# Performance work log

Measured on AMD Instinct MI355X. Metric: run time of the kernel, lower is better.

Reference implementation:

```python
import jax, jax.numpy as jnp
import numpy as np

EPS = 1e-16  # matches torch_geometric softmax denominator guard


def setup_inputs() -> dict:
    E, N, D = 1_600_000, 50_000, 32
    key = jax.random.key(0)
    k1, k2, k3, k4, k5 = jax.random.split(key, 5)
    return {
        "x": jax.random.normal(k1, (E, D), dtype=jnp.float32),
        "attention_x": jax.random.normal(k2, (E, D), dtype=jnp.float32),
        "index": jax.random.randint(k3, (E,), 0, N, dtype=jnp.int32),
        "size": N,
        "W_emb": jax.random.normal(k4, (D, D), dtype=jnp.float32) / np.sqrt(D),
        "b_emb": jnp.zeros((D,), dtype=jnp.float32),
        "W_score": jax.random.normal(k5, (D, 1), dtype=jnp.float32) / np.sqrt(D),
        "b_score": jnp.zeros((1,), dtype=jnp.float32),
    }


def reference(x, attention_x, index, size, W_emb, b_emb, W_score, b_score):
    # embedding_module: per-edge linear transform -> [E, D]
    h = x @ W_emb + b_emb
    # score_module: per-edge scalar score -> [E]
    scores = (attention_x @ W_score + b_score)[:, 0]
    # segment softmax over edges sharing the same target node
    seg_max = jax.ops.segment_max(scores, index, num_segments=size)  # [N]
    ex = jnp.exp(scores - seg_max[index])                            # [E]
    denom = jax.ops.segment_sum(ex, index, num_segments=size)       # [N]
    w = ex / (denom[index] + EPS)                                    # [E]
    # weighted scatter-add aggregation -> [N, D]
    out = jax.ops.segment_sum(h * w[:, None], index, num_segments=size)
    return out
```

## Files before the change

### kernel.cpp

```cpp
#include <hip/hip_runtime.h>

#define DD 32
#define EPSF 1e-16f
#define SCAN_T 1024
#define BSH 5
#define BNODES (1 << BSH)
#define BMAX 2048
#define K3_TPB 256
#define K3_EPT 16
#define K3_EPB (K3_TPB * K3_EPT)
#define CHUNK 1536
#define CPT (CHUNK / 256)

__global__ void score_kernel(const float* __restrict__ ax,
                             const float* __restrict__ Wsf,
                             const float* __restrict__ bsf,
                             float* __restrict__ ex, int E) {
    int i = blockIdx.x * blockDim.x + threadIdx.x;
    int e0 = i * 2;
    if (e0 >= E) return;
    bool two = (e0 + 1 < E);
    int e1 = two ? e0 + 1 : e0;

    const float4* r0 = reinterpret_cast<const float4*>(ax + (size_t)e0 * DD);
    const float4* r1 = reinterpret_cast<const float4*>(ax + (size_t)e1 * DD);
    float b = bsf[0];
    float s0 = b, s1 = b;
#pragma unroll
    for (int q = 0; q < 8; ++q) {
        float4 f0 = r0[q];
        float4 f1 = r1[q];
        float w0 = Wsf[4 * q], w1 = Wsf[4 * q + 1];
        float w2 = Wsf[4 * q + 2], w3 = Wsf[4 * q + 3];
        s0 = fmaf(f0.x, w0, s0); s0 = fmaf(f0.y, w1, s0);
        s0 = fmaf(f0.z, w2, s0); s0 = fmaf(f0.w, w3, s0);
        s1 = fmaf(f1.x, w0, s1); s1 = fmaf(f1.y, w1, s1);
        s1 = fmaf(f1.z, w2, s1); s1 = fmaf(f1.w, w3, s1);
    }
    float ex0 = __expf(s0), ex1 = __expf(s1);
    if (two) reinterpret_cast<float2*>(ex)[i] = make_float2(ex0, ex1);
    else     ex[e0] = ex0;
}

__launch_bounds__(K3_TPB)
__global__ void hist_kernel(const int* __restrict__ index,
                            int* __restrict__ bcnt, int E, int B) {
    __shared__ int lcnt[BMAX];
    int t = threadIdx.x;
    int base = blockIdx.x * K3_EPB;
    int nE = min(K3_EPB, E - base);

    for (int b = t; b < B; b += K3_TPB) lcnt[b] = 0;
    __syncthreads();
    for (int off = t; off < nE; off += K3_TPB)
        atomicAdd(&lcnt[index[base + off] >> BSH], 1);
    __syncthreads();
    for (int b = t; b < B; b += K3_TPB)
        if (lcnt[b]) atomicAdd(&bcnt[b], lcnt[b]);
}

__global__ void scan_kernel(const int* __restrict__ bcnt, int* __restrict__ boff,
                            int* __restrict__ bcursor, int B) {
    __shared__ int part[SCAN_T];
    int t = threadIdx.x;
    int chunk = (B + SCAN_T - 1) / SCAN_T;
    int lo = t * chunk;
    int hi = min(lo + chunk, B);
    int s = 0;
    for (int i = lo; i < hi; ++i) s += bcnt[i];
    part[t] = s;
    __syncthreads();
    for (int d = 1; d < SCAN_T; d <<= 1) {
        int v = (t >= d) ? part[t - d] : 0;
        __syncthreads();
        part[t] += v;
        __syncthreads();
    }
    int run = (t == 0) ? 0 : part[t - 1];
    for (int i = lo; i < hi; ++i) {
        boff[i] = run;
        bcursor[i] = run;
        run += bcnt[i];
    }
    if (t == SCAN_T - 1) boff[B] = run;
}

__launch_bounds__(K3_TPB)
__global__ void bin_kernel(const int* __restrict__ index,
                           const float* __restrict__ ex,
                           int* __restrict__ bcursor,
                           uint2* __restrict__ pairs, int E, int B) {
    __shared__ int lcnt[BMAX];
    __shared__ int lbase[BMAX];
    int t = threadIdx.x;
    int base = blockIdx.x * K3_EPB;
    int nE = min(K3_EPB, E - base);

    for (int b = t; b < B; b += K3_TPB) lcnt[b] = 0;
    __syncthreads();

    int idxv[K3_EPT];
#pragma unroll
    for (int i = 0; i < K3_EPT; ++i) {
        int off = i * K3_TPB + t;
        idxv[i] = -1;
        if (off < nE) {
            idxv[i] = index[base + off];
            atomicAdd(&lcnt[idxv[i] >> BSH], 1);
        }
    }
    __syncthreads();

    for (int b = t; b < B; b += K3_TPB) {
        int c = lcnt[b];
        lbase[b] = (c > 0) ? atomicAdd(&bcursor[b], c) : 0;
        lcnt[b] = 0;
    }
    __syncthreads();

#pragma unroll
    for (int i = 0; i < K3_EPT; ++i) {
        int off = i * K3_TPB + t;
        if (off >= nE) continue;
        int e = base + off;
        float exv = ex[e];
        int idx = idxv[i];
        int b = idx >> BSH;
        int pos = atomicAdd(&lcnt[b], 1);
        pairs[lbase[b] + pos] =
            make_uint2((unsigned)e | ((unsigned)(idx & (BNODES - 1)) << 21),
                       __float_as_uint(exv));
    }
}

__launch_bounds__(256)
__global__ void aggregate_kernel(const float* __restrict__ x,
                                 const uint2* __restrict__ pairs,
                                 const int* __restrict__ boff,
                                 const float* __restrict__ Wf,
                                 const float* __restrict__ bfv,
                                 float* __restrict__ out, int N) {
    __shared__ uint2 sp[CHUNK];
    __shared__ int cnt[BNODES];
    __shared__ int offs[BNODES + 1];
    __shared__ int cur[BNODES];

    int bk = blockIdx.x;
    int nbase = bk << BSH;
    int t = threadIdx.x;
    int wid = t >> 6;
    int lane = t & 63;
    int half = lane >> 5;
    int k = lane & 31;

    int beg = boff[bk], end = boff[bk + 1];

    float yacc[8], dacc[8];
#pragma unroll
    for (int s = 0; s < 8; ++s) { yacc[s] = 0.0f; dacc[s] = 0.0f; }

    for (int cb = beg; cb < end; cb += CHUNK) {
        int csz = min(CHUNK, end - cb);

        uint2 vreg[CPT];
#pragma unroll
        for (int j = 0; j < CPT; ++j) {
            int i = j * 256 + t;
            vreg[j].x = 0xFFFFFFFFu;
            if (i < csz) vreg[j] = pairs[cb + i];
        }

        if (t < BNODES) cnt[t] = 0;
        __syncthreads();
#pragma unroll
        for (int j = 0; j < CPT; ++j)
            if (vreg[j].x != 0xFFFFFFFFu)
                atomicAdd(&cnt[(vreg[j].x >> 21) & (BNODES - 1)], 1);
        __syncthreads();
        if (t == 0) {
            int r = 0;
            for (int n = 0; n < BNODES; ++n) { offs[n] = r; cur[n] = r; r += cnt[n]; }
            offs[BNODES] = r;
        }
        __syncthreads();
#pragma unroll
        for (int j = 0; j < CPT; ++j) {
            if (vreg[j].x != 0xFFFFFFFFu) {
                int nl = (vreg[j].x >> 21) & (BNODES - 1);
                int slot = atomicAdd(&cur[nl], 1);
                sp[slot] = vreg[j];
            }
        }
        __syncthreads();

#pragma unroll
        for (int s = 0; s < 8; ++s) {
            int nl = wid * 8 + s;
            int lo = offs[nl], hi = offs[nl + 1];
            float ya = 0.0f, da = 0.0f;
            int p = lo + half;
            for (; p + 14 < hi; p += 16) {
                uint2 a0 = sp[p],      a1 = sp[p + 2];
                uint2 a2 = sp[p + 4],  a3 = sp[p + 6];
                uint2 a4 = sp[p + 8],  a5 = sp[p + 10];
                uint2 a6 = sp[p + 12], a7 = sp[p + 14];
                float w0 = __uint_as_float(a0.y), w1 = __uint_as_float(a1.y);
                float w2 = __uint_as_float(a2.y), w3 = __uint_as_float(a3.y);
                float w4 = __uint_as_float(a4.y), w5 = __uint_as_float(a5.y);
                float w6 = __uint_as_float(a6.y), w7 = __uint_as_float(a7.y);
                float x0 = x[(size_t)(a0.x & 0x1FFFFFu) * DD + k];
                float x1 = x[(size_t)(a1.x & 0x1FFFFFu) * DD + k];
                float x2 = x[(size_t)(a2.x & 0x1FFFFFu) * DD + k];
                float x3 = x[(size_t)(a3.x & 0x1FFFFFu) * DD + k];
                float x4 = x[(size_t)(a4.x & 0x1FFFFFu) * DD + k];
                float x5 = x[(size_t)(a5.x & 0x1FFFFFu) * DD + k];
                float x6 = x[(size_t)(a6.x & 0x1FFFFFu) * DD + k];
                float x7 = x[(size_t)(a7.x & 0x1FFFFFu) * DD + k];
                ya = fmaf(w0, x0, ya); ya = fmaf(w1, x1, ya);
                ya = fmaf(w2, x2, ya); ya = fmaf(w3, x3, ya);
                ya = fmaf(w4, x4, ya); ya = fmaf(w5, x5, ya);
                ya = fmaf(w6, x6, ya); ya = fmaf(w7, x7, ya);
                da += ((w0 + w1) + (w2 + w3)) + ((w4 + w5) + (w6 + w7));
            }
            for (; p + 6 < hi; p += 8) {
                uint2 a0 = sp[p],     a1 = sp[p + 2];
                uint2 a2 = sp[p + 4], a3 = sp[p + 6];
                float w0 = __uint_as_float(a0.y), w1 = __uint_as_float(a1.y);
                float w2 = __uint_as_float(a2.y), w3 = __uint_as_float(a3.y);
                float x0 = x[(size_t)(a0.x & 0x1FFFFFu) * DD + k];
                float x1 = x[(size_t)(a1.x & 0x1FFFFFu) * DD + k];
                float x2 = x[(size_t)(a2.x & 0x1FFFFFu) * DD + k];
                float x3 = x[(size_t)(a3.x & 0x1FFFFFu) * DD + k];
                ya = fmaf(w0, x0, ya); ya = fmaf(w1, x1, ya);
                ya = fmaf(w2, x2, ya); ya = fmaf(w3, x3, ya);
                da += (w0 + w1) + (w2 + w3);
            }
            for (; p < hi; p += 2) {
                uint2 a = sp[p];
                float w = __uint_as_float(a.y);
                ya = fmaf(w, x[(size_t)(a.x & 0x1FFFFFu) * DD + k], ya);
                da += w;
            }
            yacc[s] += ya;
            dacc[s] += da;
        }
        __syncthreads();
    }

#pragma unroll
    for (int s = 0; s < 8; ++s) {
        float ya = yacc[s] + __shfl_xor(yacc[s], 32);
        float da = dacc[s] + __shfl_xor(dacc[s], 32);
        int node = nbase + wid * 8 + s;
        if (node < N) {
            float inv = 1.0f / (da + EPSF);
            float yn = ya * inv;
            float sw = da * inv;
            float o = sw * bfv[k];
#pragma unroll
            for (int kk = 0; kk < DD; ++kk)
                o = fmaf(__shfl(yn, kk), Wf[kk * DD + k], o);
            if (half == 0) out[(size_t)node * DD + k] = o;
        }
    }
}

extern "C" void kernel_launch(void* const* d_in, const int* in_sizes, int n_in,
                              void* d_out, int out_size, void* d_ws, size_t ws_size,
                              hipStream_t stream) {
    const float* x       = (const float*)d_in[0];
    const float* ax      = (const float*)d_in[1];
    const int*   index   = (const int*)d_in[2];
    const float* W_emb   = (const float*)d_in[4];
    const float* b_emb   = (const float*)d_in[5];
    const float* W_score = (const float*)d_in[6];
    const float* b_score = (const float*)d_in[7];

    int E = in_sizes[0] / DD;
    int N = out_size / DD;
    int B = (N + BNODES - 1) >> BSH;

    uint2* pairs   = (uint2*)d_ws;
    float* ex      = (float*)(pairs + (size_t)E);
    int*   bcnt    = (int*)(ex + (size_t)E);
    int*   boff    = bcnt + B;
    int*   bcursor = boff + B + 1;

    hipMemsetAsync(bcnt, 0, sizeof(int) * (size_t)B, stream);

    int blocksE2 = ((E + 1) / 2 + 255) / 256;
    score_kernel<<<blocksE2, 256, 0, stream>>>(ax, W_score, b_score, ex, E);

    int blocksK = (E + K3_EPB - 1) / K3_EPB;
    hist_kernel<<<blocksK, K3_TPB, 0, stream>>>(index, bcnt, E, B);
    scan_kernel<<<1, SCAN_T, 0, stream>>>(bcnt, boff, bcursor, B);
    bin_kernel<<<blocksK, K3_TPB, 0, stream>>>(index, ex, bcursor, pairs, E, B);
    aggregate_kernel<<<B, 256, 0, stream>>>(x, pairs, boff, W_emb, b_emb,
                                            (float*)d_out, N);
}
```

Before: 184.6 us.

## Fuse score and histogram kernels; replace serial bucket prefix with wave scan

Merges the per-edge score/exp computation with the bucket histogram into one kernel, with each thread handling four consecutive edges. This removes a launch and an extra pass over the index array. The single-thread 32-entry prefix sum in the aggregate kernel becomes a shuffle-based scan across 32 lanes. In exchange, each thread now reads strided float4 rows (four edges per thread, non-coalesced across lanes), and every 1024-edge block must zero and flush a 2048-entry shared histogram, which means many more global atomics than the old 4096-edge blocks.

```diff
diff --git a/kernel.cpp b/kernel.cpp
--- a/kernel.cpp
+++ b/kernel.cpp
@@ -11,51 +11,72 @@
 #define K3_EPB (K3_TPB * K3_EPT)
 #define CHUNK 1536
 #define CPT (CHUNK / 256)
-
-__global__ void score_kernel(const float* __restrict__ ax,
-                             const float* __restrict__ Wsf,
-                             const float* __restrict__ bsf,
-                             float* __restrict__ ex, int E) {
-    int i = blockIdx.x * blockDim.x + threadIdx.x;
-    int e0 = i * 2;
-    if (e0 >= E) return;
-    bool two = (e0 + 1 < E);
-    int e1 = two ? e0 + 1 : e0;
-
-    const float4* r0 = reinterpret_cast<const float4*>(ax + (size_t)e0 * DD);
-    const float4* r1 = reinterpret_cast<const float4*>(ax + (size_t)e1 * DD);
-    float b = bsf[0];
-    float s0 = b, s1 = b;
-#pragma unroll
-    for (int q = 0; q < 8; ++q) {
-        float4 f0 = r0[q];
-        float4 f1 = r1[q];
-        float w0 = Wsf[4 * q], w1 = Wsf[4 * q + 1];
-        float w2 = Wsf[4 * q + 2], w3 = Wsf[4 * q + 3];
-        s0 = fmaf(f0.x, w0, s0); s0 = fmaf(f0.y, w1, s0);
-        s0 = fmaf(f0.z, w2, s0); s0 = fmaf(f0.w, w3, s0);
-        s1 = fmaf(f1.x, w0, s1); s1 = fmaf(f1.y, w1, s1);
-        s1 = fmaf(f1.z, w2, s1); s1 = fmaf(f1.w, w3, s1);
-    }
-    float ex0 = __expf(s0), ex1 = __expf(s1);
-    if (two) reinterpret_cast<float2*>(ex)[i] = make_float2(ex0, ex1);
-    else     ex[e0] = ex0;
-}
-
-__launch_bounds__(K3_TPB)
-__global__ void hist_kernel(const int* __restrict__ index,
-                            int* __restrict__ bcnt, int E, int B) {
+#define S_EPT 4
+
+__launch_bounds__(256)
+__global__ void score_hist_kernel(const float* __restrict__ ax,
+                                  const int* __restrict__ index,
+                                  const float* __restrict__ Wsf,
+                                  const float* __restrict__ bsf,
+                                  float* __restrict__ ex,
+                                  int* __restrict__ bcnt, int E, int B) {
     __shared__ int lcnt[BMAX];
     int t = threadIdx.x;
-    int base = blockIdx.x * K3_EPB;
-    int nE = min(K3_EPB, E - base);
-
-    for (int b = t; b < B; b += K3_TPB) lcnt[b] = 0;
-    __syncthreads();
-    for (int off = t; off < nE; off += K3_TPB)
-        atomicAdd(&lcnt[index[base + off] >> BSH], 1);
-    __syncthreads();
-    for (int b = t; b < B; b += K3_TPB)
+    int base = blockIdx.x * (256 * S_EPT);
+    int e0 = base + t * S_EPT;
+
+    for (int b = t; b < B; b += 256) lcnt[b] = 0;
+    __syncthreads();
+
+    if (e0 + S_EPT - 1 < E) {
+        const float4* r0 = reinterpret_cast<const float4*>(ax + (size_t)e0 * DD);
+        float b0 = bsf[0];
+        float s0 = b0, s1 = b0, s2 = b0, s3 = b0;
+#pragma unroll
+        for (int q = 0; q < 8; ++q) {
+            float w0 = Wsf[4 * q], w1 = Wsf[4 * q + 1];
+            float w2 = Wsf[4 * q + 2], w3 = Wsf[4 * q + 3];
+            float4 f0 = r0[q];
+            float4 f1 = r0[q + 8];
+            float4 f2 = r0[q + 16];
+            float4 f3 = r0[q + 24];
+            s0 = fmaf(f0.x, w0, s0); s0 = fmaf(f0.y, w1, s0);
+            s0 = fmaf(f0.z, w2, s0); s0 = fmaf(f0.w, w3, s0);
+            s1 = fmaf(f1.x, w0, s1); s1 = fmaf(f1.y, w1, s1);
+            s1 = fmaf(f1.z, w2, s1); s1 = fmaf(f1.w, w3, s1);
+            s2 = fmaf(f2.x, w0, s2); s2 = fmaf(f2.y, w1, s2);
+            s2 = fmaf(f2.z, w2, s2); s2 = fmaf(f2.w, w3, s2);
+            s3 = fmaf(f3.x, w0, s3); s3 = fmaf(f3.y, w1, s3);
+            s3 = fmaf(f3.z, w2, s3); s3 = fmaf(f3.w, w3, s3);
+        }
+        float4 exv = make_float4(__expf(s0), __expf(s1), __expf(s2), __expf(s3));
+        reinterpret_cast<float4*>(ex)[e0 / 4] = exv;
+        int i0 = index[e0],     i1 = index[e0 + 1];
+        int i2 = index[e0 + 2], i3 = index[e0 + 3];
+        atomicAdd(&lcnt[i0 >> BSH], 1);
+        atomicAdd(&lcnt[i1 >> BSH], 1);
+        atomicAdd(&lcnt[i2 >> BSH], 1);
+        atomicAdd(&lcnt[i3 >> BSH], 1);
+    } else {
+        for (int j = 0; j < S_EPT; ++j) {
+            int e = e0 + j;
+            if (e >= E) break;
+            const float4* r = reinterpret_cast<const float4*>(ax + (size_t)e * DD);
+            float s = bsf[0];
+#pragma unroll
+            for (int q = 0; q < 8; ++q) {
+                float4 f = r[q];
+                s = fmaf(f.x, Wsf[4 * q],     s);
+                s = fmaf(f.y, Wsf[4 * q + 1], s);
+                s = fmaf(f.z, Wsf[4 * q + 2], s);
+                s = fmaf(f.w, Wsf[4 * q + 3], s);
+            }
+            ex[e] = __expf(s);
+            atomicAdd(&lcnt[index[e] >> BSH], 1);
+        }
+    }
+    __syncthreads();
+    for (int b = t; b < B; b += 256)
         if (lcnt[b]) atomicAdd(&bcnt[b], lcnt[b]);
 }
 
@@ -177,10 +198,17 @@
             if (vreg[j].x != 0xFFFFFFFFu)
                 atomicAdd(&cnt[(vreg[j].x >> 21) & (BNODES - 1)], 1);
         __syncthreads();
-        if (t == 0) {
-            int r = 0;
-            for (int n = 0; n < BNODES; ++n) { offs[n] = r; cur[n] = r; r += cnt[n]; }
-            offs[BNODES] = r;
+        if (t < 32) {
+            int c = cnt[t];
+            int v = c;
+#pragma unroll
+            for (int d = 1; d < 32; d <<= 1) {
+                int u = __shfl_up(v, d, 32);
+                if (t >= d) v += u;
+            }
+            offs[t] = v - c;
+            cur[t] = v - c;
+            if (t == 31) offs[BNODES] = v;
         }
         __syncthreads();
 #pragma unroll
@@ -288,12 +316,12 @@
 
     hipMemsetAsync(bcnt, 0, sizeof(int) * (size_t)B, stream);
 
-    int blocksE2 = ((E + 1) / 2 + 255) / 256;
-    score_kernel<<<blocksE2, 256, 0, stream>>>(ax, W_score, b_score, ex, E);
+    int blocksS = (E + 256 * S_EPT - 1) / (256 * S_EPT);
+    score_hist_kernel<<<blocksS, 256, 0, stream>>>(ax, index, W_score, b_score,
+                                                   ex, bcnt, E, B);
+    scan_kernel<<<1, SCAN_T, 0, stream>>>(bcnt, boff, bcursor, B);
 
     int blocksK = (E + K3_EPB - 1) / K3_EPB;
-    hist_kernel<<<blocksK, K3_TPB, 0, stream>>>(index, bcnt, E, B);
-    scan_kernel<<<1, SCAN_T, 0, stream>>>(bcnt, boff, bcursor, B);
     bin_kernel<<<blocksK, K3_TPB, 0, stream>>>(index, ex, bcursor, pairs, E, B);
     aggregate_kernel<<<B, 256, 0, stream>>>(x, pairs, boff, W_emb, b_emb,
                                             (float*)d_out, N);
```

Measured after the change: 208.8 us. 13.1% more time.
